# Kernel tuning notes

Hardware: AMD Instinct MI355X
Metric: run time of the kernel (lower is better)

## Reference

```python
import jax, jax.numpy as jnp
import numpy as np

N_SRC, N_TGT, N_EDGES = 100000, 50000, 600000
IN_CH, OUT_CH = 128, 128
NUM_EDGE_TYPES, NUM_NODE_TYPES = 7, 4


def setup_inputs() -> dict:
    key = jax.random.key(0)
    ks = jax.random.split(key, 9)
    x_src = jax.random.normal(ks[0], (N_SRC, IN_CH), dtype=jnp.float32)
    x_target = jax.random.normal(ks[1], (N_TGT, IN_CH), dtype=jnp.float32)
    # PyG Linear: y = x @ W.T (+ b); W has shape (out, in)
    rel_w = jax.random.normal(ks[2], (NUM_EDGE_TYPES, OUT_CH, IN_CH), dtype=jnp.float32) * 0.05
    root_w = jax.random.normal(ks[3], (NUM_NODE_TYPES, OUT_CH, IN_CH), dtype=jnp.float32) * 0.05
    root_b = jax.random.normal(ks[4], (NUM_NODE_TYPES, OUT_CH), dtype=jnp.float32) * 0.05
    edge_src = jax.random.randint(ks[5], (N_EDGES,), 0, N_SRC, dtype=jnp.int32)
    edge_dst = jax.random.randint(ks[6], (N_EDGES,), 0, N_TGT, dtype=jnp.int32)
    edge_type = jax.random.randint(ks[7], (N_EDGES,), 0, NUM_EDGE_TYPES, dtype=jnp.int32)
    target_node_type = jax.random.randint(ks[8], (N_TGT,), 0, NUM_NODE_TYPES, dtype=jnp.int32)
    return {
        "x_src": x_src, "x_target": x_target,
        "rel_w": rel_w, "root_w": root_w, "root_b": root_b,
        "edge_src": edge_src, "edge_dst": edge_dst,
        "edge_type": edge_type, "target_node_type": target_node_type,
    }


def reference(x_src, x_target, rel_w, root_w, root_b,
              edge_src, edge_dst, edge_type, target_node_type):
    n_tgt = x_target.shape[0]
    num_rel = rel_w.shape[0]
    num_ntypes = root_w.shape[0]
    # Gather source features once for all edges: (E, in)
    msg = x_src[edge_src]
    out = jnp.zeros((n_tgt, rel_w.shape[1]), dtype=x_target.dtype)
    # Per-relation linear transform + scatter-MEAN over that relation's edges
    # (matches one propagate(aggr='mean') call per edge type: nodes with no
    #  incoming edges of type r contribute 0 for that relation).
    for r in range(num_rel):
        mask = (edge_type == r).astype(msg.dtype)  # (E,)
        y = (msg * mask[:, None]) @ rel_w[r].T     # (E, out)
        s = jax.ops.segment_sum(y, edge_dst, num_segments=n_tgt)
        cnt = jax.ops.segment_sum(mask, edge_dst, num_segments=n_tgt)
        out = out + s / jnp.maximum(cnt, 1.0)[:, None]
    # Per-node-type root linear (with bias), masked add
    for t in range(num_ntypes):
        m = (target_node_type == t)
        root = x_target @ root_w[t].T + root_b[t]
        out = out + jnp.where(m[:, None], root, 0.0)
    return out
```

## Files before the change

kernel.cpp:

```cpp
#include <hip/hip_runtime.h>

#define NSRC 100000
#define NTGT 50000
#define NE   600000
#define CH   128
#define NREL 7
#define NTYP 4
#define NP   (NREL * NTGT)
#define NB   ((NP + 1023) / 1024)
#define MAXBLK ((NTGT + 63) / 64)

typedef __attribute__((ext_vector_type(4))) float f32x4;
typedef __attribute__((ext_vector_type(8))) short bf16x8;
typedef unsigned int uint;
typedef unsigned short ushort;

static constexpr size_t A256(size_t x) { return (x + 255) & ~(size_t)255; }
static constexpr size_t CNT_O   = 0;
static constexpr size_t TCNT_O  = A256(CNT_O + (size_t)NP * 4);
static constexpr size_t ZERO_END= TCNT_O + 256;
static constexpr size_t BSE_O   = ZERO_END;
static constexpr size_t BSR_O   = A256(BSE_O + (size_t)NB * 4);
static constexpr size_t BBE_O   = A256(BSR_O + (size_t)NB * 4);
static constexpr size_t BBR_O   = A256(BBE_O + (size_t)NB * 4);
static constexpr size_t CUR_O   = A256(BBR_O + (size_t)NB * 4);
static constexpr size_t PLO_O   = A256(CUR_O + (size_t)NP * 4);
static constexpr size_t PN_O    = A256(PLO_O + (size_t)NP * 4);
static constexpr size_t PINV_O  = A256(PN_O + (size_t)NP * 4);
static constexpr size_t PDST_O  = A256(PINV_O + (size_t)NP * 4);
static constexpr size_t RELO_O  = A256(PDST_O + (size_t)NP * 4);
static constexpr size_t BKT_O   = A256(RELO_O + 64);
static constexpr size_t SEDGE_O = A256(BKT_O + (size_t)NTYP * NTGT * 4);
static constexpr size_t WB_O    = A256(SEDGE_O + (size_t)NE * 4);
static constexpr size_t XB_O    = A256(WB_O + (size_t)(NREL + NTYP) * CH * CH * 2);
static constexpr size_t XTB_O   = A256(XB_O + (size_t)NSRC * CH * 2);

__device__ __forceinline__ uint bfpack(float a, float b) {
  uint ua = __float_as_uint(a); ua = (ua + 0x7fff + ((ua >> 16) & 1)) >> 16;
  uint ub = __float_as_uint(b); ub = (ub + 0x7fff + ((ub >> 16) & 1)) >> 16;
  return ua | (ub << 16);
}
__device__ __forceinline__ ushort f2b(float x) {
  uint u = __float_as_uint(x);
  return (ushort)((u + 0x7fff + ((u >> 16) & 1)) >> 16);
}
__device__ __forceinline__ float bl(uint u) { return __uint_as_float(u << 16); }
__device__ __forceinline__ float bh(uint u) { return __uint_as_float(u & 0xffff0000u); }

__global__ void k_count(const int* __restrict__ edst, const int* __restrict__ etyp,
                        int* __restrict__ cnt) {
  int i = blockIdx.x * 256 + threadIdx.x;
  if (i < NE) atomicAdd(&cnt[etyp[i] * NTGT + edst[i]], 1);
}

__global__ void k_bucket(const int* __restrict__ ntyp, int* __restrict__ tcnt,
                         int* __restrict__ bucket) {
  __shared__ int lcnt[NTYP];
  __shared__ int lbase[NTYP];
  int v = blockIdx.x * 256 + threadIdx.x;
  if (threadIdx.x < NTYP) lcnt[threadIdx.x] = 0;
  __syncthreads();
  int t = 0, r = 0;
  bool ok = v < NTGT;
  if (ok) { t = ntyp[v]; r = atomicAdd(&lcnt[t], 1); }
  __syncthreads();
  if (threadIdx.x < NTYP) lbase[threadIdx.x] = atomicAdd(&tcnt[threadIdx.x], lcnt[threadIdx.x]);
  __syncthreads();
  if (ok) bucket[t * NTGT + lbase[t] + r] = v;
}

__global__ __launch_bounds__(256) void k_s1(const int* __restrict__ cnt,
                                            int* __restrict__ bsE, int* __restrict__ bsR) {
  __shared__ int sE[256], sR[256];
  int t = threadIdx.x, p0 = blockIdx.x * 1024 + t * 4;
  int e = 0, r = 0;
#pragma unroll
  for (int j = 0; j < 4; ++j) {
    int p = p0 + j;
    if (p < NP) { int c = cnt[p]; e += c; r += (c > 0); }
  }
  sE[t] = e; sR[t] = r; __syncthreads();
  for (int s = 128; s > 0; s >>= 1) {
    if (t < s) { sE[t] += sE[t + s]; sR[t] += sR[t + s]; }
    __syncthreads();
  }
  if (t == 0) { bsE[blockIdx.x] = sE[0]; bsR[blockIdx.x] = sR[0]; }
}

__global__ __launch_bounds__(512) void k_s2(const int* __restrict__ bsE, const int* __restrict__ bsR,
                                            int* __restrict__ bbE, int* __restrict__ bbR,
                                            int* __restrict__ reloff) {
  __shared__ int sE[512], sR[512];
  int t = threadIdx.x;
  int e = (t < NB) ? bsE[t] : 0;
  int r = (t < NB) ? bsR[t] : 0;
  sE[t] = e; sR[t] = r; __syncthreads();
  for (int s = 1; s < 512; s <<= 1) {
    int ae = 0, ar = 0;
    if (t >= s) { ae = sE[t - s]; ar = sR[t - s]; }
    __syncthreads();
    sE[t] += ae; sR[t] += ar;
    __syncthreads();
  }
  if (t < NB) { bbE[t] = sE[t] - e; bbR[t] = sR[t] - r; }
  if (t == NB - 1) reloff[NREL] = sR[t];
}

__global__ __launch_bounds__(256) void k_s3(const int* __restrict__ cnt,
    const int* __restrict__ bbE, const int* __restrict__ bbR,
    int* __restrict__ cur, int* __restrict__ plo, int* __restrict__ pn,
    float* __restrict__ pinv, int* __restrict__ pdst, int* __restrict__ reloff) {
  __shared__ int sE[256], sR[256];
  int t = threadIdx.x, p0 = blockIdx.x * 1024 + t * 4;
  int c[4]; int e = 0, r = 0;
#pragma unroll
  for (int j = 0; j < 4; ++j) {
    int p = p0 + j;
    c[j] = (p < NP) ? cnt[p] : 0;
    e += c[j]; r += (c[j] > 0);
  }
  sE[t] = e; sR[t] = r; __syncthreads();
  for (int s = 1; s < 256; s <<= 1) {
    int ae = 0, ar = 0;
    if (t >= s) { ae = sE[t - s]; ar = sR[t - s]; }
    __syncthreads();
    sE[t] += ae; sR[t] += ar;
    __syncthreads();
  }
  int baseE = bbE[blockIdx.x] + sE[t] - e;
  int baseR = bbR[blockIdx.x] + sR[t] - r;
#pragma unroll
  for (int j = 0; j < 4; ++j) {
    int p = p0 + j;
    if (p < NP) {
      cur[p] = baseE;
      if ((p % NTGT) == 0) reloff[p / NTGT] = baseR;
      if (c[j] > 0) {
        plo[baseR] = baseE; pn[baseR] = c[j];
        pinv[baseR] = 1.0f / (float)c[j];
        pdst[baseR] = p % NTGT;
        baseR++;
      }
      baseE += c[j];
    }
  }
}

__global__ void k_esort(const int* __restrict__ esrc, const int* __restrict__ edst,
                        const int* __restrict__ etyp, int* __restrict__ cur,
                        int* __restrict__ sedge) {
  int i = blockIdx.x * 256 + threadIdx.x;
  if (i < NE) {
    int p = etyp[i] * NTGT + edst[i];
    int pos = atomicAdd(&cur[p], 1);
    sedge[pos] = esrc[i];
  }
}

__global__ void k_conv(const float* __restrict__ xsrc, const float* __restrict__ xt,
                       const float* __restrict__ relw, const float* __restrict__ rootw,
                       ushort* __restrict__ xb, ushort* __restrict__ xtb,
                       ushort* __restrict__ wb) {
  const long long NXB = (long long)NSRC * CH / 4;
  const long long NXT = (long long)NTGT * CH / 4;
  const long long NWR = (long long)NREL * CH * CH / 4;
  const long long NWT = (long long)NTYP * CH * CH / 4;
  long long i4 = (long long)blockIdx.x * 256 + threadIdx.x;
  const float* src; ushort* dst; long long off;
  if (i4 < NXB) { src = xsrc; dst = xb; off = i4; }
  else if (i4 < NXB + NXT) { src = xt; dst = xtb; off = i4 - NXB; }
  else if (i4 < NXB + NXT + NWR) { src = relw; dst = wb; off = i4 - NXB - NXT; }
  else if (i4 < NXB + NXT + NWR + NWT) {
    src = rootw; dst = wb + (size_t)NREL * CH * CH; off = i4 - NXB - NXT - NWR;
  } else return;
  float4 v = *(const float4*)(src + off * 4);
  uint lo = (uint)f2b(v.x) | ((uint)f2b(v.y) << 16);
  uint hi = (uint)f2b(v.z) | ((uint)f2b(v.w) << 16);
  uint2 o = make_uint2(lo, hi);
  *(uint2*)(dst + off * 4) = o;
}

__global__ void k_init(const float* __restrict__ rootb, const int* __restrict__ ntyp,
                       float* __restrict__ out) {
  int idx = blockIdx.x * 256 + threadIdx.x;
  if (idx >= NTGT * 32) return;
  int v = idx >> 5, c4 = (idx & 31) << 2;
  int t = ntyp[v];
  *(float4*)(out + (size_t)v * CH + c4) = *(const float4*)(rootb + (size_t)t * CH + c4);
}

__device__ __forceinline__ void mfma_tail(const ushort* strip, const ushort* W,
                                          int m, int quad, const int* rowmap,
                                          float* __restrict__ out) {
  bf16x8 aF[4];
#pragma unroll
  for (int ks = 0; ks < 4; ++ks) {
    int c = ks * 4 + quad;
    aF[ks] = *(const bf16x8*)&strip[(m * 16 + (c ^ m)) << 3];
  }
  f32x4 acc[8];
#pragma unroll
  for (int ct = 0; ct < 8; ++ct) acc[ct] = (f32x4){0.f, 0.f, 0.f, 0.f};
#pragma unroll
  for (int ct = 0; ct < 8; ++ct) {
    int n = ct * 16 + m;
#pragma unroll
    for (int ks = 0; ks < 4; ++ks) {
      bf16x8 bF = *(const bf16x8*)(W + (size_t)n * CH + ks * 32 + quad * 8);
      acc[ct] = __builtin_amdgcn_mfma_f32_16x16x32_bf16(aF[ks], bF, acc[ct], 0, 0, 0);
    }
  }
#pragma unroll
  for (int ct = 0; ct < 8; ++ct)
#pragma unroll
    for (int reg = 0; reg < 4; ++reg)
      if (rowmap[reg] >= 0)
        unsafeAtomicAdd(&out[(size_t)rowmap[reg] * CH + ct * 16 + m], acc[ct][reg]);
}

__global__ __launch_bounds__(256) void k_mega(const ushort* __restrict__ xb,
    const ushort* __restrict__ xtb, const ushort* __restrict__ wb,
    const int* __restrict__ plo, const int* __restrict__ pn,
    const float* __restrict__ pinv, const int* __restrict__ pdst,
    const int* __restrict__ reloff, const int* __restrict__ sedge,
    const int* __restrict__ bucket, const int* __restrict__ tcnt,
    float* __restrict__ out) {
  __shared__ ushort As[4 * 16 * CH];
  int wv = threadIdx.x >> 6, ln = threadIdx.x & 63;
  ushort* strip = As + wv * (16 * CH);
  int m = ln & 15, quad = ln >> 4;
  int y = blockIdx.y;

  if (y < NREL) {
    int rel = y;
    int base = reloff[rel], relend = reloff[rel + 1];
    int row0 = blockIdx.x * 64;
    if (row0 >= relend - base) return;
    for (int i = 0; i < 16; ++i) {
      int gr = base + row0 + wv * 16 + i;
      float ax = 0.f, ay = 0.f, inv = 0.f;
      if (gr < relend) {
        int lo = plo[gr], n = pn[gr];
        inv = pinv[gr];
        const int* sp = sedge + lo;
        int q = 0;
        for (; q + 1 < n; q += 2) {
          int s0 = sp[q], s1 = sp[q + 1];
          uint u0 = *(const uint*)(xb + (size_t)s0 * CH + (ln << 1));
          uint u1 = *(const uint*)(xb + (size_t)s1 * CH + (ln << 1));
          ax += bl(u0) + bl(u1);
          ay += bh(u0) + bh(u1);
        }
        if (q < n) {
          uint u0 = *(const uint*)(xb + (size_t)sp[q] * CH + (ln << 1));
          ax += bl(u0); ay += bh(u0);
        }
      }
      uint w = bfpack(ax * inv, ay * inv);
      int c = ln >> 2;
      *(uint*)&strip[((i * 16 + (c ^ i)) << 3) + ((ln & 3) << 1)] = w;
    }
    int rowmap[4];
#pragma unroll
    for (int reg = 0; reg < 4; ++reg) {
      int gro = base + row0 + wv * 16 + quad * 4 + reg;
      rowmap[reg] = (gro < relend) ? pdst[gro] : -1;
    }
    mfma_tail(strip, wb + (size_t)rel * CH * CH, m, quad, rowmap, out);
  } else {
    int typ = y - NREL;
    int nb = tcnt[typ];
    int row0 = blockIdx.x * 64;
    if (row0 >= nb) return;
    const int* bk = bucket + (size_t)typ * NTGT;
    for (int i = 0; i < 16; ++i) {
      int rr = row0 + wv * 16 + i;
      uint w = 0;
      if (rr < nb) {
        int v = bk[rr];
        w = *(const uint*)(xtb + (size_t)v * CH + (ln << 1));
      }
      int c = ln >> 2;
      *(uint*)&strip[((i * 16 + (c ^ i)) << 3) + ((ln & 3) << 1)] = w;
    }
    int rowmap[4];
#pragma unroll
    for (int reg = 0; reg < 4; ++reg) {
      int rro = row0 + wv * 16 + quad * 4 + reg;
      rowmap[reg] = (rro < nb) ? bk[rro] : -1;
    }
    mfma_tail(strip, wb + (size_t)(NREL + typ) * CH * CH, m, quad, rowmap, out);
  }
}

extern "C" void kernel_launch(void* const* d_in, const int* in_sizes, int n_in,
                              void* d_out, int out_size, void* d_ws, size_t ws_size,
                              hipStream_t stream) {
  (void)in_sizes; (void)n_in; (void)out_size; (void)ws_size;
  const float* xsrc  = (const float*)d_in[0];
  const float* xt    = (const float*)d_in[1];
  const float* relw  = (const float*)d_in[2];
  const float* rootw = (const float*)d_in[3];
  const float* rootb = (const float*)d_in[4];
  const int* esrc = (const int*)d_in[5];
  const int* edst = (const int*)d_in[6];
  const int* etyp = (const int*)d_in[7];
  const int* ntyp = (const int*)d_in[8];
  float* out = (float*)d_out;

  char* ws = (char*)d_ws;
  int*   cnt    = (int*)(ws + CNT_O);
  int*   tcnt   = (int*)(ws + TCNT_O);
  int*   bsE    = (int*)(ws + BSE_O);
  int*   bsR    = (int*)(ws + BSR_O);
  int*   bbE    = (int*)(ws + BBE_O);
  int*   bbR    = (int*)(ws + BBR_O);
  int*   cur    = (int*)(ws + CUR_O);
  int*   plo    = (int*)(ws + PLO_O);
  int*   pn     = (int*)(ws + PN_O);
  float* pinv   = (float*)(ws + PINV_O);
  int*   pdst   = (int*)(ws + PDST_O);
  int*   reloff = (int*)(ws + RELO_O);
  int*   bucket = (int*)(ws + BKT_O);
  int*   sedge  = (int*)(ws + SEDGE_O);
  ushort* wb    = (ushort*)(ws + WB_O);
  ushort* xb    = (ushort*)(ws + XB_O);
  ushort* xtb   = (ushort*)(ws + XTB_O);

  hipMemsetAsync(ws, 0, ZERO_END, stream);
  k_count<<<dim3((NE + 255) / 256), dim3(256), 0, stream>>>(edst, etyp, cnt);
  k_bucket<<<dim3((NTGT + 255) / 256), dim3(256), 0, stream>>>(ntyp, tcnt, bucket);
  k_s1<<<dim3(NB), dim3(256), 0, stream>>>(cnt, bsE, bsR);
  k_s2<<<dim3(1), dim3(512), 0, stream>>>(bsE, bsR, bbE, bbR, reloff);
  k_s3<<<dim3(NB), dim3(256), 0, stream>>>(cnt, bbE, bbR, cur, plo, pn, pinv, pdst, reloff);
  k_esort<<<dim3((NE + 255) / 256), dim3(256), 0, stream>>>(esrc, edst, etyp, cur, sedge);
  {
    long long tot4 = (long long)NSRC * CH / 4 + (long long)NTGT * CH / 4 +
                     (long long)(NREL + NTYP) * CH * CH / 4;
    k_conv<<<dim3((unsigned)((tot4 + 255) / 256)), dim3(256), 0, stream>>>(
        xsrc, xt, relw, rootw, xb, xtb, wb);
  }
  k_init<<<dim3((NTGT * 32 + 255) / 256), dim3(256), 0, stream>>>(rootb, ntyp, out);
  k_mega<<<dim3(MAXBLK, NREL + NTYP), dim3(256), 0, stream>>>(
      xb, xtb, wb, plo, pn, pinv, pdst, reloff, sedge, bucket, tcnt, out);
}
```

Before: 413.5 us.

## Edge-parallel gather with LDS atomic accumulation and fused preprocessing launches

Replaces the per-row gather loop in the relation path with an edge-parallel scheme. Each wave takes batches of 32 sorted edges, broadcasts source and local row indices via readlane, and accumulates into a 64x128 fp32 LDS tile with atomic adds, using a new per-edge row-index array. This removes load imbalance from varying in-degree and the serial dependent loads per row. It costs LDS float atomics and a larger shared buffer (32KB), which may reduce occupancy. It also merges conv/count/bucket and esort/init into two combined launches to cut launch overhead.

New measurement: 641.5 us. 55.1% more time.

```diff
diff --git a/kernel.cpp b/kernel.cpp
--- a/kernel.cpp
+++ b/kernel.cpp
@@ -14,6 +14,15 @@
 typedef __attribute__((ext_vector_type(8))) short bf16x8;
 typedef unsigned int uint;
 typedef unsigned short ushort;
+
+static constexpr long long NXB4 = (long long)NSRC * CH / 4;
+static constexpr long long NXT4 = (long long)NTGT * CH / 4;
+static constexpr long long NWR4 = (long long)NREL * CH * CH / 4;
+static constexpr long long NWT4 = (long long)NTYP * CH * CH / 4;
+static constexpr int CONVB  = (int)((NXB4 + NXT4 + NWR4 + NWT4 + 255) / 256);
+static constexpr int COUNTB = (NE + 255) / 256;
+static constexpr int BUCKETB= (NTGT + 255) / 256;
+static constexpr int INITB  = (NTGT * 32 + 255) / 256;
 
 static constexpr size_t A256(size_t x) { return (x + 255) & ~(size_t)255; }
 static constexpr size_t CNT_O   = 0;
@@ -34,6 +43,8 @@
 static constexpr size_t WB_O    = A256(SEDGE_O + (size_t)NE * 4);
 static constexpr size_t XB_O    = A256(WB_O + (size_t)(NREL + NTYP) * CH * CH * 2);
 static constexpr size_t XTB_O   = A256(XB_O + (size_t)NSRC * CH * 2);
+static constexpr size_t PRK_O   = A256(XTB_O + (size_t)NTGT * CH * 2);
+static constexpr size_t EPAIR_O = A256(PRK_O + (size_t)NP * 4);
 
 __device__ __forceinline__ uint bfpack(float a, float b) {
   uint ua = __float_as_uint(a); ua = (ua + 0x7fff + ((ua >> 16) & 1)) >> 16;
@@ -47,26 +58,50 @@
 __device__ __forceinline__ float bl(uint u) { return __uint_as_float(u << 16); }
 __device__ __forceinline__ float bh(uint u) { return __uint_as_float(u & 0xffff0000u); }
 
-__global__ void k_count(const int* __restrict__ edst, const int* __restrict__ etyp,
-                        int* __restrict__ cnt) {
-  int i = blockIdx.x * 256 + threadIdx.x;
-  if (i < NE) atomicAdd(&cnt[etyp[i] * NTGT + edst[i]], 1);
-}
-
-__global__ void k_bucket(const int* __restrict__ ntyp, int* __restrict__ tcnt,
-                         int* __restrict__ bucket) {
+__global__ __launch_bounds__(256) void k_pre1(
+    const float* __restrict__ xsrc, const float* __restrict__ xt,
+    const float* __restrict__ relw, const float* __restrict__ rootw,
+    ushort* __restrict__ xb, ushort* __restrict__ xtb, ushort* __restrict__ wb,
+    const int* __restrict__ edst, const int* __restrict__ etyp, int* __restrict__ cnt,
+    const int* __restrict__ ntyp, int* __restrict__ tcnt, int* __restrict__ bucket) {
   __shared__ int lcnt[NTYP];
   __shared__ int lbase[NTYP];
-  int v = blockIdx.x * 256 + threadIdx.x;
-  if (threadIdx.x < NTYP) lcnt[threadIdx.x] = 0;
-  __syncthreads();
-  int t = 0, r = 0;
-  bool ok = v < NTGT;
-  if (ok) { t = ntyp[v]; r = atomicAdd(&lcnt[t], 1); }
-  __syncthreads();
-  if (threadIdx.x < NTYP) lbase[threadIdx.x] = atomicAdd(&tcnt[threadIdx.x], lcnt[threadIdx.x]);
-  __syncthreads();
-  if (ok) bucket[t * NTGT + lbase[t] + r] = v;
+  int bx = blockIdx.x;
+  if (bx < CONVB) {
+    long long i4 = (long long)bx * 256 + threadIdx.x;
+    const float* src; ushort* dst; long long off;
+    if (i4 < NXB4) { src = xsrc; dst = xb; off = i4; }
+    else if (i4 < NXB4 + NXT4) { src = xt; dst = xtb; off = i4 - NXB4; }
+    else if (i4 < NXB4 + NXT4 + NWR4) { src = relw; dst = wb; off = i4 - NXB4 - NXT4; }
+    else if (i4 < NXB4 + NXT4 + NWR4 + NWT4) {
+      src = rootw; dst = wb + (size_t)NREL * CH * CH; off = i4 - NXB4 - NXT4 - NWR4;
+    } else return;
+    float4 v = *(const float4*)(src + off * 4);
+    uint lo = (uint)f2b(v.x) | ((uint)f2b(v.y) << 16);
+    uint hi = (uint)f2b(v.z) | ((uint)f2b(v.w) << 16);
+    uint2 o = make_uint2(lo, hi);
+    *(uint2*)(dst + off * 4) = o;
+    return;
+  }
+  bx -= CONVB;
+  if (bx < COUNTB) {
+    int i = bx * 256 + threadIdx.x;
+    if (i < NE) atomicAdd(&cnt[etyp[i] * NTGT + edst[i]], 1);
+    return;
+  }
+  bx -= COUNTB;
+  {
+    int v = bx * 256 + threadIdx.x;
+    if (threadIdx.x < NTYP) lcnt[threadIdx.x] = 0;
+    __syncthreads();
+    int t = 0, r = 0;
+    bool ok = v < NTGT;
+    if (ok) { t = ntyp[v]; r = atomicAdd(&lcnt[t], 1); }
+    __syncthreads();
+    if (threadIdx.x < NTYP) lbase[threadIdx.x] = atomicAdd(&tcnt[threadIdx.x], lcnt[threadIdx.x]);
+    __syncthreads();
+    if (ok) bucket[t * NTGT + lbase[t] + r] = v;
+  }
 }
 
 __global__ __launch_bounds__(256) void k_s1(const int* __restrict__ cnt,
@@ -109,7 +144,8 @@
 __global__ __launch_bounds__(256) void k_s3(const int* __restrict__ cnt,
     const int* __restrict__ bbE, const int* __restrict__ bbR,
     int* __restrict__ cur, int* __restrict__ plo, int* __restrict__ pn,
-    float* __restrict__ pinv, int* __restrict__ pdst, int* __restrict__ reloff) {
+    float* __restrict__ pinv, int* __restrict__ pdst, int* __restrict__ reloff,
+    int* __restrict__ prk) {
   __shared__ int sE[256], sR[256];
   int t = threadIdx.x, p0 = blockIdx.x * 1024 + t * 4;
   int c[4]; int e = 0, r = 0;
@@ -139,6 +175,7 @@
         plo[baseR] = baseE; pn[baseR] = c[j];
         pinv[baseR] = 1.0f / (float)c[j];
         pdst[baseR] = p % NTGT;
+        prk[p] = baseR;
         baseR++;
       }
       baseE += c[j];
@@ -146,43 +183,25 @@
   }
 }
 
-__global__ void k_esort(const int* __restrict__ esrc, const int* __restrict__ edst,
-                        const int* __restrict__ etyp, int* __restrict__ cur,
-                        int* __restrict__ sedge) {
-  int i = blockIdx.x * 256 + threadIdx.x;
-  if (i < NE) {
-    int p = etyp[i] * NTGT + edst[i];
-    int pos = atomicAdd(&cur[p], 1);
-    sedge[pos] = esrc[i];
-  }
-}
-
-__global__ void k_conv(const float* __restrict__ xsrc, const float* __restrict__ xt,
-                       const float* __restrict__ relw, const float* __restrict__ rootw,
-                       ushort* __restrict__ xb, ushort* __restrict__ xtb,
-                       ushort* __restrict__ wb) {
-  const long long NXB = (long long)NSRC * CH / 4;
-  const long long NXT = (long long)NTGT * CH / 4;
-  const long long NWR = (long long)NREL * CH * CH / 4;
-  const long long NWT = (long long)NTYP * CH * CH / 4;
-  long long i4 = (long long)blockIdx.x * 256 + threadIdx.x;
-  const float* src; ushort* dst; long long off;
-  if (i4 < NXB) { src = xsrc; dst = xb; off = i4; }
-  else if (i4 < NXB + NXT) { src = xt; dst = xtb; off = i4 - NXB; }
-  else if (i4 < NXB + NXT + NWR) { src = relw; dst = wb; off = i4 - NXB - NXT; }
-  else if (i4 < NXB + NXT + NWR + NWT) {
-    src = rootw; dst = wb + (size_t)NREL * CH * CH; off = i4 - NXB - NXT - NWR;
-  } else return;
-  float4 v = *(const float4*)(src + off * 4);
-  uint lo = (uint)f2b(v.x) | ((uint)f2b(v.y) << 16);
-  uint hi = (uint)f2b(v.z) | ((uint)f2b(v.w) << 16);
-  uint2 o = make_uint2(lo, hi);
-  *(uint2*)(dst + off * 4) = o;
-}
-
-__global__ void k_init(const float* __restrict__ rootb, const int* __restrict__ ntyp,
-                       float* __restrict__ out) {
-  int idx = blockIdx.x * 256 + threadIdx.x;
+__global__ __launch_bounds__(256) void k_pre2(
+    const int* __restrict__ esrc, const int* __restrict__ edst,
+    const int* __restrict__ etyp, int* __restrict__ cur,
+    const int* __restrict__ prk, int* __restrict__ sedge, int* __restrict__ epair,
+    const float* __restrict__ rootb, const int* __restrict__ ntyp,
+    float* __restrict__ out) {
+  int bx = blockIdx.x;
+  if (bx < COUNTB) {
+    int i = bx * 256 + threadIdx.x;
+    if (i < NE) {
+      int p = etyp[i] * NTGT + edst[i];
+      int pos = atomicAdd(&cur[p], 1);
+      sedge[pos] = esrc[i];
+      epair[pos] = prk[p];
+    }
+    return;
+  }
+  bx -= COUNTB;
+  int idx = bx * 256 + threadIdx.x;
   if (idx >= NTGT * 32) return;
   int v = idx >> 5, c4 = (idx & 31) << 2;
   int t = ntyp[v];
@@ -220,12 +239,13 @@
 
 __global__ __launch_bounds__(256) void k_mega(const ushort* __restrict__ xb,
     const ushort* __restrict__ xtb, const ushort* __restrict__ wb,
-    const int* __restrict__ plo, const int* __restrict__ pn,
-    const float* __restrict__ pinv, const int* __restrict__ pdst,
-    const int* __restrict__ reloff, const int* __restrict__ sedge,
+    const int* __restrict__ plo, const float* __restrict__ pinv,
+    const int* __restrict__ pdst, const int* __restrict__ reloff,
+    const int* __restrict__ sedge, const int* __restrict__ epair,
     const int* __restrict__ bucket, const int* __restrict__ tcnt,
     float* __restrict__ out) {
-  __shared__ ushort As[4 * 16 * CH];
+  __shared__ float accs[64 * CH];
+  ushort* As = (ushort*)accs;
   int wv = threadIdx.x >> 6, ln = threadIdx.x & 63;
   ushort* strip = As + wv * (16 * CH);
   int m = ln & 15, quad = ln >> 4;
@@ -236,34 +256,61 @@
     int base = reloff[rel], relend = reloff[rel + 1];
     int row0 = blockIdx.x * 64;
     if (row0 >= relend - base) return;
-    for (int i = 0; i < 16; ++i) {
-      int gr = base + row0 + wv * 16 + i;
-      float ax = 0.f, ay = 0.f, inv = 0.f;
-      if (gr < relend) {
-        int lo = plo[gr], n = pn[gr];
-        inv = pinv[gr];
-        const int* sp = sedge + lo;
-        int q = 0;
-        for (; q + 1 < n; q += 2) {
-          int s0 = sp[q], s1 = sp[q + 1];
-          uint u0 = *(const uint*)(xb + (size_t)s0 * CH + (ln << 1));
-          uint u1 = *(const uint*)(xb + (size_t)s1 * CH + (ln << 1));
-          ax += bl(u0) + bl(u1);
-          ay += bh(u0) + bh(u1);
+    int gr0 = base + row0;
+    int gr1 = gr0 + 64; if (gr1 > relend) gr1 = relend;
+    int nrtot = reloff[NREL];
+    int estart = plo[gr0];
+    int eend = (gr1 < nrtot) ? plo[gr1] : NE;
+
+#pragma unroll
+    for (int i = 0; i < 32; ++i) accs[threadIdx.x + i * 256] = 0.f;
+    __syncthreads();
+
+    for (int b0 = estart + wv * 32; b0 < eend; b0 += 128) {
+      int sv = 0, rv = 0;
+      int e = b0 + (ln & 31);
+      if (ln < 32 && e < eend) { sv = sedge[e]; rv = epair[e] - gr0; }
+      int nb = eend - b0; if (nb > 32) nb = 32;
+      if (nb == 32) {
+#pragma unroll
+        for (int j = 0; j < 32; ++j) {
+          int s = __builtin_amdgcn_readlane(sv, j);
+          int row = __builtin_amdgcn_readlane(rv, j);
+          uint u = *(const uint*)(xb + (size_t)s * CH + (ln << 1));
+          atomicAdd(&accs[row * CH + (ln << 1)], bl(u));
+          atomicAdd(&accs[row * CH + (ln << 1) + 1], bh(u));
         }
-        if (q < n) {
-          uint u0 = *(const uint*)(xb + (size_t)sp[q] * CH + (ln << 1));
-          ax += bl(u0); ay += bh(u0);
+      } else {
+        for (int j = 0; j < nb; ++j) {
+          int s = __shfl(sv, j);
+          int row = __shfl(rv, j);
+          uint u = *(const uint*)(xb + (size_t)s * CH + (ln << 1));
+          atomicAdd(&accs[row * CH + (ln << 1)], bl(u));
+          atomicAdd(&accs[row * CH + (ln << 1) + 1], bh(u));
         }
       }
-      uint w = bfpack(ax * inv, ay * inv);
+    }
+    __syncthreads();
+
+    uint wpk[16];
+#pragma unroll
+    for (int i = 0; i < 16; ++i) {
+      int r = wv * 16 + i;
+      int gr = gr0 + r;
+      float inv = (gr < relend) ? pinv[gr] : 0.f;
+      float2 a = *(const float2*)&accs[r * CH + (ln << 1)];
+      wpk[i] = bfpack(a.x * inv, a.y * inv);
+    }
+    __syncthreads();
+#pragma unroll
+    for (int i = 0; i < 16; ++i) {
       int c = ln >> 2;
-      *(uint*)&strip[((i * 16 + (c ^ i)) << 3) + ((ln & 3) << 1)] = w;
+      *(uint*)&strip[((i * 16 + (c ^ i)) << 3) + ((ln & 3) << 1)] = wpk[i];
     }
     int rowmap[4];
 #pragma unroll
     for (int reg = 0; reg < 4; ++reg) {
-      int gro = base + row0 + wv * 16 + quad * 4 + reg;
+      int gro = gr0 + wv * 16 + quad * 4 + reg;
       rowmap[reg] = (gro < relend) ? pdst[gro] : -1;
     }
     mfma_tail(strip, wb + (size_t)rel * CH * CH, m, quad, rowmap, out);
@@ -326,21 +373,18 @@
   ushort* wb    = (ushort*)(ws + WB_O);
   ushort* xb    = (ushort*)(ws + XB_O);
   ushort* xtb   = (ushort*)(ws + XTB_O);
+  int*   prk    = (int*)(ws + PRK_O);
+  int*   epair  = (int*)(ws + EPAIR_O);
 
   hipMemsetAsync(ws, 0, ZERO_END, stream);
-  k_count<<<dim3((NE + 255) / 256), dim3(256), 0, stream>>>(edst, etyp, cnt);
-  k_bucket<<<dim3((NTGT + 255) / 256), dim3(256), 0, stream>>>(ntyp, tcnt, bucket);
+  k_pre1<<<dim3(CONVB + COUNTB + BUCKETB), dim3(256), 0, stream>>>(
+      xsrc, xt, relw, rootw, xb, xtb, wb, edst, etyp, cnt, ntyp, tcnt, bucket);
   k_s1<<<dim3(NB), dim3(256), 0, stream>>>(cnt, bsE, bsR);
   k_s2<<<dim3(1), dim3(512), 0, stream>>>(bsE, bsR, bbE, bbR, reloff);
-  k_s3<<<dim3(NB), dim3(256), 0, stream>>>(cnt, bbE, bbR, cur, plo, pn, pinv, pdst, reloff);
-  k_esort<<<dim3((NE + 255) / 256), dim3(256), 0, stream>>>(esrc, edst, etyp, cur, sedge);
-  {
-    long long tot4 = (long long)NSRC * CH / 4 + (long long)NTGT * CH / 4 +
-                     (long long)(NREL + NTYP) * CH * CH / 4;
-    k_conv<<<dim3((unsigned)((tot4 + 255) / 256)), dim3(256), 0, stream>>>(
-        xsrc, xt, relw, rootw, xb, xtb, wb);
-  }
-  k_init<<<dim3((NTGT * 32 + 255) / 256), dim3(256), 0, stream>>>(rootb, ntyp, out);
+  k_s3<<<dim3(NB), dim3(256), 0, stream>>>(cnt, bbE, bbR, cur, plo, pn, pinv, pdst,
+                                           reloff, prk);
+  k_pre2<<<dim3(COUNTB + INITB), dim3(256), 0, stream>>>(
+      esrc, edst, etyp, cur, prk, sedge, epair, rootb, ntyp, out);
   k_mega<<<dim3(MAXBLK, NREL + NTYP), dim3(256), 0, stream>>>(
-      xb, xtb, wb, plo, pn, pinv, pdst, reloff, sedge, bucket, tcnt, out);
-}
+      xb, xtb, wb, plo, pinv, pdst, reloff, sedge, epair, bucket, tcnt, out);
+}
```
